# Kernel tuning notes

Measured on AMD Instinct MI355X. Metric: run time of the kernel, lower is better.

The kernel has to match this reference:

```python
import jax, jax.numpy as jnp
import numpy as np

B, H, W, C = 64, 224, 224, 3
P = 16
DIM = 768
DEPTH = 12
NH, DH = 12, 64
FF = 3072
NPATCH = (H // P) * (W // P)   # 196
L = NPATCH + 1                 # 197 tokens (CLS + patches)
KEEP = int(L * (1.0 - 0.75))   # 49 unmasked tokens


def setup_inputs() -> dict:
    key = jax.random.key(0)
    ks = jax.random.split(key, 16)
    s = 0.02
    inp = {
        'inputs': jax.random.normal(ks[0], (B, H, W, C), jnp.float32),
        'conv_w': jax.random.normal(ks[1], (P, P, C, DIM), jnp.float32) * s,
        'ct':     jax.random.normal(ks[2], (1, 1, DIM), jnp.float32) * s,
        'pe':     jax.random.normal(ks[3], (1, L, DIM), jnp.float32) * s,
        'ln1_s': jnp.ones((DEPTH, DIM), jnp.float32),
        'ln1_b': jnp.zeros((DEPTH, DIM), jnp.float32),
        'qkv_w': jax.random.normal(ks[4], (DEPTH, DIM, 3 * NH * DH), jnp.float32) * s,
        'proj_w': jax.random.normal(ks[5], (DEPTH, NH * DH, DIM), jnp.float32) * s,
        'ln2_s': jnp.ones((DEPTH, DIM), jnp.float32),
        'ln2_b': jnp.zeros((DEPTH, DIM), jnp.float32),
        'w1': jax.random.normal(ks[6], (DEPTH, DIM, FF), jnp.float32) * s,
        'b1': jnp.zeros((DEPTH, FF), jnp.float32),
        'w2': jax.random.normal(ks[7], (DEPTH, FF, DIM), jnp.float32) * s,
        'b2': jnp.zeros((DEPTH, DIM), jnp.float32),
        # Faithful to original: permutation of arange(1, L+1); max value 197
        # is out-of-range and gets clamped by JAX gather, exactly as upstream.
        'mask_idx': jax.random.permutation(ks[8], jnp.arange(1, L + 1))[:KEEP].astype(jnp.int32),
    }
    return inp


def _layernorm(x, scale, bias, eps=1e-9):
    m = jnp.mean(x, axis=-1, keepdims=True)
    v = jnp.var(x, axis=-1, keepdims=True)
    return (x - m) * jax.lax.rsqrt(v + eps) * scale + bias


def _encoder(x, layer_params):
    # x: [B, KEEP, DIM]; layer_params leaves stacked on axis 0 (DEPTH)
    inv_sqrt_d = 1.0 / jnp.sqrt(jnp.float32(DH))

    def block(x, p):
        ln1s, ln1b, qw, pw, ln2s, ln2b, w1, b1, w2, b2 = p
        h = _layernorm(x, ln1s, ln1b)
        qkv = h @ qw                                   # [B, Lk, 3*NH*DH]
        q, k, v = jnp.split(qkv, 3, axis=-1)
        def heads(t):
            return t.reshape(x.shape[0], -1, NH, DH).transpose(0, 2, 1, 3)
        q, k, v = heads(q), heads(k), heads(v)         # [B, NH, Lk, DH]
        att = jax.nn.softmax(jnp.einsum('bhqd,bhkd->bhqk', q, k) * inv_sqrt_d)
        o = jnp.einsum('bhqk,bhkd->bhqd', att, v)
        o = o.transpose(0, 2, 1, 3).reshape(x.shape[0], -1, NH * DH) @ pw
        x = x + o
        h2 = _layernorm(x, ln2s, ln2b)
        x = x + (jax.nn.gelu(h2 @ w1 + b1) @ w2 + b2)
        return x, None

    x, _ = jax.lax.scan(block, x, layer_params)
    return x


def reference(inputs, conv_w, ct, pe, ln1_s, ln1_b, qkv_w, proj_w,
              ln2_s, ln2_b, w1, b1, w2, b2, mask_idx):
    # patch embed: stride-P conv, no bias
    out = jax.lax.conv_general_dilated(
        inputs, conv_w, window_strides=(P, P), padding='VALID',
        dimension_numbers=('NHWC', 'HWIO', 'NHWC'))      # [B, 14, 14, DIM]
    out = out.reshape(out.shape[0], -1, out.shape[3])     # [B, 196, DIM]
    out = jnp.concatenate((jnp.repeat(ct, out.shape[0], axis=0), out), axis=1)
    out = out + pe                                        # [B, 197, DIM]
    patches = out[:, mask_idx]                            # [B, 49, DIM]
    layer_params = (ln1_s, ln1_b, qkv_w, proj_w, ln2_s, ln2_b, w1, b1, w2, b2)
    return _encoder(patches, layer_params)
```

## Files before the change

### kernel.cpp

```cpp
#include <hip/hip_runtime.h>
#include <hip/hip_bf16.h>
#include <math.h>

#define DIMV   768
#define BATCH  64
#define KEEPT  49
#define MTOK   (BATCH*KEEPT)
#define NHEADS 12
#define DHEAD  64
#define FFV    3072
#define NDEPTH 12

typedef short short8 __attribute__((ext_vector_type(8)));
typedef float floatx4 __attribute__((ext_vector_type(4)));
typedef unsigned short ushort;

__device__ __forceinline__ ushort f2bf(float f) {
  __hip_bfloat16 h = __float2bfloat16(f);
  return *(ushort*)&h;
}

__device__ __forceinline__ void async_cp16(const void* g, void* l) {
  __builtin_amdgcn_global_load_lds((const __attribute__((address_space(1))) void*)g,
                                   (__attribute__((address_space(3))) void*)l,
                                   16, 0, 0);
}

__global__ __launch_bounds__(256) void gather_patches(
    const float* __restrict__ inp, const int* __restrict__ mask,
    __hip_bfloat16* __restrict__ apix)
{
  int gid = blockIdx.x * 256 + threadIdx.x;
  if (gid >= MTOK * DIMV) return;
  int r = gid / DIMV, k = gid - r * DIMV;
  int b = r / KEEPT, t = r - b * KEEPT;
  int j = mask[t];
  j = j < 0 ? 0 : (j > 196 ? 196 : j);
  float v = 0.f;
  if (j > 0) {
    int p  = j - 1, py = p / 14, px = p - py * 14;
    int ky = k / 48, rem = k - ky * 48, kx = rem / 3, c = rem - kx * 3;
    v = inp[(((b * 224) + py * 16 + ky) * 224 + px * 16 + kx) * 3 + c];
  }
  apix[gid] = __float2bfloat16(v);
}

__global__ __launch_bounds__(256) void finish_embed(
    float* __restrict__ x, const float* __restrict__ ct,
    const float* __restrict__ pe, const int* __restrict__ mask)
{
  int gid = blockIdx.x * 256 + threadIdx.x;
  if (gid >= MTOK * DIMV) return;
  int r = gid / DIMV, d = gid - r * DIMV;
  int t = r % KEEPT;
  int j = mask[t];
  j = j < 0 ? 0 : (j > 196 ? 196 : j);
  float base = (j == 0) ? ct[d] : x[gid];
  x[gid] = base + pe[j * DIMV + d];
}

__global__ __launch_bounds__(256) void layernorm_k(
    const float* __restrict__ x, const float* __restrict__ sc,
    const float* __restrict__ bi, __hip_bfloat16* __restrict__ out)
{
  __shared__ float red[8];
  int r = blockIdx.x;
  const float* xr = x + (size_t)r * DIMV;
  int t = threadIdx.x;
  float v[3];
  float s = 0.f, ss = 0.f;
#pragma unroll
  for (int i = 0; i < 3; i++) {
    float a = xr[t + i * 256];
    v[i] = a; s += a; ss += a * a;
  }
#pragma unroll
  for (int off = 32; off > 0; off >>= 1) {
    s  += __shfl_down(s,  off, 64);
    ss += __shfl_down(ss, off, 64);
  }
  int wave = t >> 6, lane = t & 63;
  if (lane == 0) { red[wave] = s; red[4 + wave] = ss; }
  __syncthreads();
  if (t == 0) {
    float a  = red[0] + red[1] + red[2] + red[3];
    float b2 = red[4] + red[5] + red[6] + red[7];
    float m  = a * (1.f / DIMV);
    float var = b2 * (1.f / DIMV) - m * m;
    red[0] = m;
    red[1] = rsqrtf(var + 1e-9f);
  }
  __syncthreads();
  float m = red[0], rs = red[1];
  __hip_bfloat16* outr = out + (size_t)r * DIMV;
#pragma unroll
  for (int i = 0; i < 3; i++) {
    int d = t + i * 256;
    outr[d] = __float2bfloat16((v[i] - m) * rs * sc[d] + bi[d]);
  }
}

__device__ __forceinline__ void transpose_tile64(
    const float* __restrict__ src, __hip_bfloat16* __restrict__ dst,
    int R, int C, int tr, int tcc)
{
  __shared__ float lds[64][65];
  const int tid = threadIdx.x;
  const int r0 = tr * 64, c0 = tcc * 64;
  const int lr = tid >> 4, lc4 = (tid & 15) * 4;
#pragma unroll
  for (int p = 0; p < 4; p++) {
    float4 v = *(const float4*)(src + (size_t)(r0 + p * 16 + lr) * C + c0 + lc4);
    lds[p * 16 + lr][lc4 + 0] = v.x;
    lds[p * 16 + lr][lc4 + 1] = v.y;
    lds[p * 16 + lr][lc4 + 2] = v.z;
    lds[p * 16 + lr][lc4 + 3] = v.w;
  }
  __syncthreads();
#pragma unroll
  for (int p = 0; p < 4; p++) {
    int c  = p * 16 + (tid >> 4);
    int rc = (tid & 15) * 4;
    ushort4 ov;
    ov.x = f2bf(lds[rc + 0][c]);
    ov.y = f2bf(lds[rc + 1][c]);
    ov.z = f2bf(lds[rc + 2][c]);
    ov.w = f2bf(lds[rc + 3][c]);
    *(ushort4*)((ushort*)dst + (size_t)(c0 + c) * R + r0 + rc) = ov;
  }
}

__global__ __launch_bounds__(256) void transpose_one(
    const float* __restrict__ src, __hip_bfloat16* __restrict__ dst, int R, int C)
{
  int tc = C >> 6;
  transpose_tile64(src, dst, R, C, blockIdx.x / tc, blockIdx.x % tc);
}

#define QKV_TE  ((size_t)2304*768)
#define PROJ_TE ((size_t)768*768)
#define W1_TE   ((size_t)3072*768)
#define W2_TE   ((size_t)768*3072)
#define LSTRIDE (QKV_TE + PROJ_TE + W1_TE + W2_TE)

__global__ __launch_bounds__(256) void convert_weights(
    const float* __restrict__ qkv_w, const float* __restrict__ proj_w,
    const float* __restrict__ w1, const float* __restrict__ w2,
    __hip_bfloat16* __restrict__ dstBase, int layer0, size_t dstStride)
{
  int l = layer0 + blockIdx.y;
  __hip_bfloat16* d = dstBase + (size_t)blockIdx.y * dstStride;
  int tile = blockIdx.x;
  const float* src; __hip_bfloat16* dst; int R, C, t0;
  if (tile < 432)       { src = qkv_w  + (size_t)l*768*2304; dst = d;                          R=768;  C=2304; t0=tile; }
  else if (tile < 576)  { src = proj_w + (size_t)l*768*768;  dst = d + QKV_TE;                 R=768;  C=768;  t0=tile-432; }
  else if (tile < 1152) { src = w1     + (size_t)l*768*3072; dst = d + QKV_TE+PROJ_TE;         R=768;  C=3072; t0=tile-576; }
  else                  { src = w2     + (size_t)l*3072*768; dst = d + QKV_TE+PROJ_TE+W1_TE;   R=3072; C=768;  t0=tile-1152; }
  int tc = C >> 6;
  transpose_tile64(src, dst, R, C, t0 / tc, t0 % tc);
}

enum { EPI_NONE = 0, EPI_RESID = 1, EPI_BIAS_GELU = 2, EPI_BIAS_RESID = 3 };

template <int TN, int EPI, bool OUT_BF16>
__global__ __launch_bounds__(256) void gemm_mfma(
    const ushort* __restrict__ A, const ushort* __restrict__ Bt,
    const float* __restrict__ Cin, const float* __restrict__ bias,
    void* __restrict__ Cout, int M, int N, int K)
{
  constexpr int AM = (TN == 128) ? 4 : 2;
  constexpr int B_LOADS = TN / 64;
  __shared__ ushort As[128 * 32];
  __shared__ ushort Bs[TN * 32];

  const int tid  = threadIdx.x;
  const int wave = tid >> 6, lane = tid & 63;
  const int bm = blockIdx.y, bn = blockIdx.x;

  const int wm0 = (TN == 128) ? (wave & 1) * 64 : wave * 32;
  const int wn0 = (TN == 128) ? (wave >> 1) * 64 : 0;

  floatx4 acc[AM][4];
#pragma unroll
  for (int i = 0; i < AM; i++)
#pragma unroll
    for (int j = 0; j < 4; j++) { floatx4 z = {0.f,0.f,0.f,0.f}; acc[i][j] = z; }

  const int lrow = lane >> 2, lchunk = (lane & 3) * 8;
  const ushort* aSrc[2];
  ushort*       aDst[2];
#pragma unroll
  for (int i = 0; i < 2; i++) {
    int row = bm * 128 + (wave * 2 + i) * 16 + lrow;
    row = row < M - 1 ? row : M - 1;
    aSrc[i] = A + (size_t)row * K + lchunk;
    aDst[i] = As + (wave * 2 + i) * 512;
  }
  const ushort* bSrc[B_LOADS];
  ushort*       bDst[B_LOADS];
#pragma unroll
  for (int i = 0; i < B_LOADS; i++) {
    int row = bn * TN + (wave * B_LOADS + i) * 16 + lrow;
    bSrc[i] = Bt + (size_t)row * K + lchunk;
    bDst[i] = Bs + (wave * B_LOADS + i) * 512;
  }

  for (int k0 = 0; k0 < K; k0 += 32) {
    __syncthreads();
#pragma unroll
    for (int i = 0; i < 2; i++)       async_cp16(aSrc[i] + k0, aDst[i]);
#pragma unroll
    for (int i = 0; i < B_LOADS; i++) async_cp16(bSrc[i] + k0, bDst[i]);
    __syncthreads();

    short8 af[AM], bf[4];
#pragma unroll
    for (int mt = 0; mt < AM; mt++)
      af[mt] = *(const short8*)&As[(wm0 + mt * 16 + (lane & 15)) * 32 + (lane >> 4) * 8];
#pragma unroll
    for (int nt = 0; nt < 4; nt++)
      bf[nt] = *(const short8*)&Bs[(wn0 + nt * 16 + (lane & 15)) * 32 + (lane >> 4) * 8];
#pragma unroll
    for (int mt = 0; mt < AM; mt++)
#pragma unroll
      for (int nt = 0; nt < 4; nt++)
        acc[mt][nt] = __builtin_amdgcn_mfma_f32_16x16x32_bf16(af[mt], bf[nt], acc[mt][nt], 0, 0, 0);
  }

  const int colb = bn * TN + wn0 + (lane & 15);
  const int rq   = (lane >> 4) * 4;
#pragma unroll
  for (int mt = 0; mt < AM; mt++) {
#pragma unroll
    for (int r = 0; r < 4; r++) {
      int row = bm * 128 + wm0 + mt * 16 + rq + r;
      if (row >= M) continue;
#pragma unroll
      for (int nt = 0; nt < 4; nt++) {
        int col = colb + nt * 16;
        float u = acc[mt][nt][r];
        if (EPI == EPI_BIAS_GELU || EPI == EPI_BIAS_RESID) u += bias[col];
        if (EPI == EPI_BIAS_GELU) {
          float t3 = u * u * u;
          u = 0.5f * u * (1.f + tanhf(0.7978845608028654f * (u + 0.044715f * t3)));
        }
        if (EPI == EPI_RESID || EPI == EPI_BIAS_RESID) u += Cin[(size_t)row * N + col];
        if (OUT_BF16)
          ((__hip_bfloat16*)Cout)[(size_t)row * N + col] = __float2bfloat16(u);
        else
          ((float*)Cout)[(size_t)row * N + col] = u;
      }
    }
  }
}

__global__ __launch_bounds__(64) void attn_mfma(
    const ushort* __restrict__ qkv, ushort* __restrict__ o)
{
  __shared__ ushort qA[64 * 72];
  __shared__ ushort kB[64 * 72];
  __shared__ ushort vT[64 * 72];
  __shared__ ushort pA[64 * 72];
  const int b = blockIdx.x, hh = blockIdx.y;
  const int lane = threadIdx.x;
  const int fr = lane & 15, fc = lane >> 4;

  const ushort* base = qkv + (size_t)b * KEEPT * (3 * DIMV) + hh * 64;
  for (int r = 0; r < KEEPT; r++) {
    const ushort* row = base + (size_t)r * (3 * DIMV);
    qA[r * 72 + lane] = row[lane];
    kB[r * 72 + lane] = row[DIMV + lane];
    vT[lane * 72 + r] = row[2 * DIMV + lane];
  }
#pragma unroll
  for (int r = KEEPT; r < 64; r++) {
    qA[r * 72 + lane] = 0;
    kB[r * 72 + lane] = 0;
    vT[lane * 72 + r] = 0;
  }
  __syncthreads();

  floatx4 sacc[4][4];
#pragma unroll
  for (int mt = 0; mt < 4; mt++)
#pragma unroll
    for (int nt = 0; nt < 4; nt++) { floatx4 z = {0.f,0.f,0.f,0.f}; sacc[mt][nt] = z; }

#pragma unroll
  for (int kk = 0; kk < 2; kk++) {
    const int ch = kk * 32 + fc * 8;
    short8 af[4], bf[4];
#pragma unroll
    for (int mt = 0; mt < 4; mt++) af[mt] = *(const short8*)&qA[(mt * 16 + fr) * 72 + ch];
#pragma unroll
    for (int nt = 0; nt < 4; nt++) bf[nt] = *(const short8*)&kB[(nt * 16 + fr) * 72 + ch];
#pragma unroll
    for (int mt = 0; mt < 4; mt++)
#pragma unroll
      for (int nt = 0; nt < 4; nt++)
        sacc[mt][nt] = __builtin_amdgcn_mfma_f32_16x16x32_bf16(af[mt], bf[nt], sacc[mt][nt], 0, 0, 0);
  }

  float inv[4][4];
#pragma unroll
  for (int mt = 0; mt < 4; mt++) {
#pragma unroll
    for (int r = 0; r < 4; r++) {
      float mx = -1e30f;
#pragma unroll
      for (int nt = 0; nt < 4; nt++) {
        float s = sacc[mt][nt][r] * 0.125f;
        if (nt == 3 && fr >= 1) s = -1e30f;
        sacc[mt][nt][r] = s;
        mx = fmaxf(mx, s);
      }
      mx = fmaxf(mx, __shfl_xor(mx, 1, 64));
      mx = fmaxf(mx, __shfl_xor(mx, 2, 64));
      mx = fmaxf(mx, __shfl_xor(mx, 4, 64));
      mx = fmaxf(mx, __shfl_xor(mx, 8, 64));
      float sum = 0.f;
#pragma unroll
      for (int nt = 0; nt < 4; nt++) {
        float e = __expf(sacc[mt][nt][r] - mx);
        sacc[mt][nt][r] = e;
        sum += e;
      }
      sum += __shfl_xor(sum, 1, 64);
      sum += __shfl_xor(sum, 2, 64);
      sum += __shfl_xor(sum, 4, 64);
      sum += __shfl_xor(sum, 8, 64);
      inv[mt][r] = 1.f / sum;
    }
  }

#pragma unroll
  for (int mt = 0; mt < 4; mt++)
#pragma unroll
    for (int r = 0; r < 4; r++)
#pragma unroll
      for (int nt = 0; nt < 4; nt++)
        pA[(mt * 16 + fc * 4 + r) * 72 + nt * 16 + fr] = f2bf(sacc[mt][nt][r]);
  __syncthreads();

  floatx4 oacc[4][4];
#pragma unroll
  for (int mt = 0; mt < 4; mt++)
#pragma unroll
    for (int nt = 0; nt < 4; nt++) { floatx4 z = {0.f,0.f,0.f,0.f}; oacc[mt][nt] = z; }

#pragma unroll
  for (int kk = 0; kk < 2; kk++) {
    const int ch = kk * 32 + fc * 8;
    short8 af[4], bf[4];
#pragma unroll
    for (int mt = 0; mt < 4; mt++) af[mt] = *(const short8*)&pA[(mt * 16 + fr) * 72 + ch];
#pragma unroll
    for (int nt = 0; nt < 4; nt++) bf[nt] = *(const short8*)&vT[(nt * 16 + fr) * 72 + ch];
#pragma unroll
    for (int mt = 0; mt < 4; mt++)
#pragma unroll
      for (int nt = 0; nt < 4; nt++)
        oacc[mt][nt] = __builtin_amdgcn_mfma_f32_16x16x32_bf16(af[mt], bf[nt], oacc[mt][nt], 0, 0, 0);
  }

  ushort* obase = o + (size_t)b * KEEPT * DIMV + hh * 64;
#pragma unroll
  for (int mt = 0; mt < 4; mt++)
#pragma unroll
    for (int r = 0; r < 4; r++) {
      int q = mt * 16 + fc * 4 + r;
      if (q < KEEPT) {
#pragma unroll
        for (int nt = 0; nt < 4; nt++)
          obase[(size_t)q * DIMV + nt * 16 + fr] = f2bf(oacc[mt][nt][r] * inv[mt][r]);
      }
    }
}

extern "C" void kernel_launch(void* const* d_in, const int* in_sizes, int n_in,
                              void* d_out, int out_size, void* d_ws, size_t ws_size,
                              hipStream_t stream)
{
  (void)in_sizes; (void)n_in; (void)out_size;
  const float* inputs = (const float*)d_in[0];
  const float* conv_w = (const float*)d_in[1];
  const float* ct     = (const float*)d_in[2];
  const float* pe     = (const float*)d_in[3];
  const float* ln1_s  = (const float*)d_in[4];
  const float* ln1_b  = (const float*)d_in[5];
  const float* qkv_w  = (const float*)d_in[6];
  const float* proj_w = (const float*)d_in[7];
  const float* ln2_s  = (const float*)d_in[8];
  const float* ln2_b  = (const float*)d_in[9];
  const float* w1     = (const float*)d_in[10];
  const float* b1     = (const float*)d_in[11];
  const float* w2     = (const float*)d_in[12];
  const float* b2     = (const float*)d_in[13];
  const int*   mask   = (const int*)d_in[14];
  float* out = (float*)d_out;

  char* wsb = (char*)d_ws;
  float*          x     = (float*)wsb;
  __hip_bfloat16* h     = (__hip_bfloat16*)(wsb + 9633792);
  __hip_bfloat16* big   = (__hip_bfloat16*)(wsb + 9633792 + 4816896);
  __hip_bfloat16* convT = (__hip_bfloat16*)(wsb + 9633792 + 4816896 + 19267584);
  __hip_bfloat16* wbuf  = (__hip_bfloat16*)(wsb + 9633792 + 4816896 + 19267584 + 1179648);
  const size_t base_bytes = 9633792ull + 4816896 + 19267584 + 1179648;
  const bool all_mode = ws_size >= base_bytes + 12ull * LSTRIDE * 2;

  __hip_bfloat16* apix = h;
  __hip_bfloat16* qkv  = big;
  __hip_bfloat16* g    = big;

  dim3 blk(256);
  const int nelem = MTOK * DIMV;
  const int nblk  = (nelem + 255) / 256;
  const int mg    = (MTOK + 127) / 128;

  transpose_one<<<144, blk, 0, stream>>>(conv_w, convT, 768, 768);
  if (all_mode)
    convert_weights<<<dim3(1728, 12), blk, 0, stream>>>(
        qkv_w, proj_w, w1, w2, wbuf, 0, LSTRIDE);

  gather_patches<<<nblk, blk, 0, stream>>>(inputs, mask, apix);
  gemm_mfma<64, EPI_NONE, false><<<dim3(12, mg), blk, 0, stream>>>(
      (const ushort*)apix, (const ushort*)convT, nullptr, nullptr, x,
      MTOK, DIMV, DIMV);
  finish_embed<<<nblk, blk, 0, stream>>>(x, ct, pe, mask);

  for (int l = 0; l < NDEPTH; l++) {
    __hip_bfloat16* wl = wbuf + (all_mode ? (size_t)l * LSTRIDE : 0);
    if (!all_mode)
      convert_weights<<<dim3(1728, 1), blk, 0, stream>>>(
          qkv_w, proj_w, w1, w2, wbuf, l, 0);
    const ushort* qkvT  = (const ushort*)wl;
    const ushort* projT = (const ushort*)(wl + QKV_TE);
    const ushort* w1T   = (const ushort*)(wl + QKV_TE + PROJ_TE);
    const ushort* w2T   = (const ushort*)(wl + QKV_TE + PROJ_TE + W1_TE);

    layernorm_k<<<MTOK, blk, 0, stream>>>(x, ln1_s + l * DIMV, ln1_b + l * DIMV, h);
    gemm_mfma<128, EPI_NONE, true><<<dim3(18, mg), blk, 0, stream>>>(
        (const ushort*)h, qkvT, nullptr, nullptr, qkv, MTOK, 3 * DIMV, DIMV);
    attn_mfma<<<dim3(BATCH, NHEADS), dim3(64), 0, stream>>>(
        (const ushort*)qkv, (ushort*)h);
    gemm_mfma<64, EPI_RESID, false><<<dim3(12, mg), blk, 0, stream>>>(
        (const ushort*)h, projT, x, nullptr, x, MTOK, DIMV, DIMV);
    layernorm_k<<<MTOK, blk, 0, stream>>>(x, ln2_s + l * DIMV, ln2_b + l * DIMV, h);
    gemm_mfma<128, EPI_BIAS_GELU, true><<<dim3(24, mg), blk, 0, stream>>>(
        (const ushort*)h, w1T, nullptr, b1 + (size_t)l * FFV, g, MTOK, FFV, DIMV);
    float* dst = (l == NDEPTH - 1) ? out : x;
    gemm_mfma<64, EPI_BIAS_RESID, false><<<dim3(12, mg), blk, 0, stream>>>(
        (const ushort*)g, w2T, x, b2 + (size_t)l * DIMV, dst, MTOK, DIMV, FFV);
  }
}
```

Baseline: 2.492 ms.

## Split attention across four waves, fuse embed epilogue, widen transpose stores

The attention kernel now runs 256 threads per (batch, head) block. Each wave owns 16 query rows, and Q/K are loaded into LDS with vectorized 16-byte loads, which is meant to raise occupancy and cut serial per-lane loads. The finish_embed pass is folded into the patch-embedding GEMM epilogue (CLS/pos-embed add), removing one full read/write of x and a launch. The weight transpose now writes 16-byte vectors instead of 8-byte ones, at the cost of more strided LDS column reads per thread.

```diff
diff --git a/kernel.cpp b/kernel.cpp
--- a/kernel.cpp
+++ b/kernel.cpp
@@ -14,6 +14,7 @@
 typedef short short8 __attribute__((ext_vector_type(8)));
 typedef float floatx4 __attribute__((ext_vector_type(4)));
 typedef unsigned short ushort;
+typedef unsigned short ushortx8 __attribute__((ext_vector_type(8)));
 
 __device__ __forceinline__ ushort f2bf(float f) {
   __hip_bfloat16 h = __float2bfloat16(f);
@@ -45,20 +46,6 @@
   apix[gid] = __float2bfloat16(v);
 }
 
-__global__ __launch_bounds__(256) void finish_embed(
-    float* __restrict__ x, const float* __restrict__ ct,
-    const float* __restrict__ pe, const int* __restrict__ mask)
-{
-  int gid = blockIdx.x * 256 + threadIdx.x;
-  if (gid >= MTOK * DIMV) return;
-  int r = gid / DIMV, d = gid - r * DIMV;
-  int t = r % KEEPT;
-  int j = mask[t];
-  j = j < 0 ? 0 : (j > 196 ? 196 : j);
-  float base = (j == 0) ? ct[d] : x[gid];
-  x[gid] = base + pe[j * DIMV + d];
-}
-
 __global__ __launch_bounds__(256) void layernorm_k(
     const float* __restrict__ x, const float* __restrict__ sc,
     const float* __restrict__ bi, __hip_bfloat16* __restrict__ out)
@@ -117,17 +104,15 @@
     lds[p * 16 + lr][lc4 + 3] = v.w;
   }
   __syncthreads();
-#pragma unroll
-  for (int p = 0; p < 4; p++) {
-    int c  = p * 16 + (tid >> 4);
-    int rc = (tid & 15) * 4;
-    ushort4 ov;
-    ov.x = f2bf(lds[rc + 0][c]);
-    ov.y = f2bf(lds[rc + 1][c]);
-    ov.z = f2bf(lds[rc + 2][c]);
-    ov.w = f2bf(lds[rc + 3][c]);
-    *(ushort4*)((ushort*)dst + (size_t)(c0 + c) * R + r0 + rc) = ov;
-  }
+  const int c = tid >> 2, rc = (tid & 3) * 8;
+  ushortx8 o0, o1;
+#pragma unroll
+  for (int j = 0; j < 8; j++) o0[j] = f2bf(lds[rc + j][c]);
+#pragma unroll
+  for (int j = 0; j < 8; j++) o1[j] = f2bf(lds[rc + 32 + j][c]);
+  ushort* drow = (ushort*)dst + (size_t)(c0 + c) * R + r0;
+  *(ushortx8*)(drow + rc)      = o0;
+  *(ushortx8*)(drow + rc + 32) = o1;
 }
 
 __global__ __launch_bounds__(256) void transpose_one(
@@ -160,12 +145,14 @@
   transpose_tile64(src, dst, R, C, t0 / tc, t0 % tc);
 }
 
-enum { EPI_NONE = 0, EPI_RESID = 1, EPI_BIAS_GELU = 2, EPI_BIAS_RESID = 3 };
+enum { EPI_NONE = 0, EPI_RESID = 1, EPI_BIAS_GELU = 2, EPI_BIAS_RESID = 3,
+       EPI_EMBED = 4 };
 
 template <int TN, int EPI, bool OUT_BF16>
 __global__ __launch_bounds__(256) void gemm_mfma(
     const ushort* __restrict__ A, const ushort* __restrict__ Bt,
     const float* __restrict__ Cin, const float* __restrict__ bias,
+    const float* __restrict__ pe, const int* __restrict__ mask,
     void* __restrict__ Cout, int M, int N, int K)
 {
   constexpr int AM = (TN == 128) ? 4 : 2;
@@ -245,6 +232,13 @@
           u = 0.5f * u * (1.f + tanhf(0.7978845608028654f * (u + 0.044715f * t3)));
         }
         if (EPI == EPI_RESID || EPI == EPI_BIAS_RESID) u += Cin[(size_t)row * N + col];
+        if (EPI == EPI_EMBED) {
+          int t = row % KEEPT;
+          int j = mask[t];
+          j = j < 0 ? 0 : (j > 196 ? 196 : j);
+          if (j == 0) u = bias[col];
+          u += pe[(size_t)j * DIMV + col];
+        }
         if (OUT_BF16)
           ((__hip_bfloat16*)Cout)[(size_t)row * N + col] = __float2bfloat16(u);
         else
@@ -254,7 +248,7 @@
   }
 }
 
-__global__ __launch_bounds__(64) void attn_mfma(
+__global__ __launch_bounds__(256) void attn_mfma(
     const ushort* __restrict__ qkv, ushort* __restrict__ o)
 {
   __shared__ ushort qA[64 * 72];
@@ -262,119 +256,110 @@
   __shared__ ushort vT[64 * 72];
   __shared__ ushort pA[64 * 72];
   const int b = blockIdx.x, hh = blockIdx.y;
-  const int lane = threadIdx.x;
+  const int tid = threadIdx.x;
+  const int wave = tid >> 6, lane = tid & 63;
   const int fr = lane & 15, fc = lane >> 4;
 
   const ushort* base = qkv + (size_t)b * KEEPT * (3 * DIMV) + hh * 64;
-  for (int r = 0; r < KEEPT; r++) {
-    const ushort* row = base + (size_t)r * (3 * DIMV);
-    qA[r * 72 + lane] = row[lane];
-    kB[r * 72 + lane] = row[DIMV + lane];
-    vT[lane * 72 + r] = row[2 * DIMV + lane];
-  }
-#pragma unroll
-  for (int r = KEEPT; r < 64; r++) {
-    qA[r * 72 + lane] = 0;
-    kB[r * 72 + lane] = 0;
-    vT[lane * 72 + r] = 0;
+
+#pragma unroll
+  for (int it = 0; it < 2; it++) {
+    int r  = it * 32 + wave * 8 + (lane >> 3);
+    int cc = (lane & 7) * 8;
+    short8 qv = {0,0,0,0,0,0,0,0};
+    short8 kv = {0,0,0,0,0,0,0,0};
+    if (r < KEEPT) {
+      const ushort* row = base + (size_t)r * (3 * DIMV);
+      qv = *(const short8*)(row + cc);
+      kv = *(const short8*)(row + DIMV + cc);
+    }
+    *(short8*)&qA[r * 72 + cc] = qv;
+    *(short8*)&kB[r * 72 + cc] = kv;
+  }
+  for (int r = wave; r < 64; r += 4) {
+    ushort v = 0;
+    if (r < KEEPT) v = base[(size_t)r * (3 * DIMV) + 2 * DIMV + lane];
+    vT[lane * 72 + r] = v;
   }
   __syncthreads();
 
-  floatx4 sacc[4][4];
-#pragma unroll
-  for (int mt = 0; mt < 4; mt++)
-#pragma unroll
-    for (int nt = 0; nt < 4; nt++) { floatx4 z = {0.f,0.f,0.f,0.f}; sacc[mt][nt] = z; }
+  const int q0 = wave * 16;
+  floatx4 sacc[4];
+#pragma unroll
+  for (int nt = 0; nt < 4; nt++) { floatx4 z = {0.f,0.f,0.f,0.f}; sacc[nt] = z; }
 
 #pragma unroll
   for (int kk = 0; kk < 2; kk++) {
     const int ch = kk * 32 + fc * 8;
-    short8 af[4], bf[4];
-#pragma unroll
-    for (int mt = 0; mt < 4; mt++) af[mt] = *(const short8*)&qA[(mt * 16 + fr) * 72 + ch];
-#pragma unroll
-    for (int nt = 0; nt < 4; nt++) bf[nt] = *(const short8*)&kB[(nt * 16 + fr) * 72 + ch];
-#pragma unroll
-    for (int mt = 0; mt < 4; mt++)
-#pragma unroll
-      for (int nt = 0; nt < 4; nt++)
-        sacc[mt][nt] = __builtin_amdgcn_mfma_f32_16x16x32_bf16(af[mt], bf[nt], sacc[mt][nt], 0, 0, 0);
-  }
-
-  float inv[4][4];
-#pragma unroll
-  for (int mt = 0; mt < 4; mt++) {
-#pragma unroll
-    for (int r = 0; r < 4; r++) {
-      float mx = -1e30f;
-#pragma unroll
-      for (int nt = 0; nt < 4; nt++) {
-        float s = sacc[mt][nt][r] * 0.125f;
-        if (nt == 3 && fr >= 1) s = -1e30f;
-        sacc[mt][nt][r] = s;
-        mx = fmaxf(mx, s);
-      }
-      mx = fmaxf(mx, __shfl_xor(mx, 1, 64));
-      mx = fmaxf(mx, __shfl_xor(mx, 2, 64));
-      mx = fmaxf(mx, __shfl_xor(mx, 4, 64));
-      mx = fmaxf(mx, __shfl_xor(mx, 8, 64));
-      float sum = 0.f;
-#pragma unroll
-      for (int nt = 0; nt < 4; nt++) {
-        float e = __expf(sacc[mt][nt][r] - mx);
-        sacc[mt][nt][r] = e;
-        sum += e;
-      }
-      sum += __shfl_xor(sum, 1, 64);
-      sum += __shfl_xor(sum, 2, 64);
-      sum += __shfl_xor(sum, 4, 64);
-      sum += __shfl_xor(sum, 8, 64);
-      inv[mt][r] = 1.f / sum;
-    }
-  }
-
-#pragma unroll
-  for (int mt = 0; mt < 4; mt++)
-#pragma unroll
-    for (int r = 0; r < 4; r++)
-#pragma unroll
-      for (int nt = 0; nt < 4; nt++)
-        pA[(mt * 16 + fc * 4 + r) * 72 + nt * 16 + fr] = f2bf(sacc[mt][nt][r]);
+    short8 af = *(const short8*)&qA[(q0 + fr) * 72 + ch];
+#pragma unroll
+    for (int nt = 0; nt < 4; nt++) {
+      short8 bf = *(const short8*)&kB[(nt * 16 + fr) * 72 + ch];
+      sacc[nt] = __builtin_amdgcn_mfma_f32_16x16x32_bf16(af, bf, sacc[nt], 0, 0, 0);
+    }
+  }
+
+  float inv[4];
+#pragma unroll
+  for (int r = 0; r < 4; r++) {
+    float mx = -1e30f;
+#pragma unroll
+    for (int nt = 0; nt < 4; nt++) {
+      float s = sacc[nt][r] * 0.125f;
+      if (nt == 3 && fr >= 1) s = -1e30f;
+      sacc[nt][r] = s;
+      mx = fmaxf(mx, s);
+    }
+    mx = fmaxf(mx, __shfl_xor(mx, 1, 64));
+    mx = fmaxf(mx, __shfl_xor(mx, 2, 64));
+    mx = fmaxf(mx, __shfl_xor(mx, 4, 64));
+    mx = fmaxf(mx, __shfl_xor(mx, 8, 64));
+    float sum = 0.f;
+#pragma unroll
+    for (int nt = 0; nt < 4; nt++) {
+      float e = __expf(sacc[nt][r] - mx);
+      sacc[nt][r] = e;
+      sum += e;
+    }
+    sum += __shfl_xor(sum, 1, 64);
+    sum += __shfl_xor(sum, 2, 64);
+    sum += __shfl_xor(sum, 4, 64);
+    sum += __shfl_xor(sum, 8, 64);
+    inv[r] = 1.f / sum;
+  }
+
+#pragma unroll
+  for (int r = 0; r < 4; r++)
+#pragma unroll
+    for (int nt = 0; nt < 4; nt++)
+      pA[(q0 + fc * 4 + r) * 72 + nt * 16 + fr] = f2bf(sacc[nt][r]);
   __syncthreads();
 
-  floatx4 oacc[4][4];
-#pragma unroll
-  for (int mt = 0; mt < 4; mt++)
-#pragma unroll
-    for (int nt = 0; nt < 4; nt++) { floatx4 z = {0.f,0.f,0.f,0.f}; oacc[mt][nt] = z; }
+  floatx4 oacc[4];
+#pragma unroll
+  for (int nt = 0; nt < 4; nt++) { floatx4 z = {0.f,0.f,0.f,0.f}; oacc[nt] = z; }
 
 #pragma unroll
   for (int kk = 0; kk < 2; kk++) {
     const int ch = kk * 32 + fc * 8;
-    short8 af[4], bf[4];
-#pragma unroll
-    for (int mt = 0; mt < 4; mt++) af[mt] = *(const short8*)&pA[(mt * 16 + fr) * 72 + ch];
-#pragma unroll
-    for (int nt = 0; nt < 4; nt++) bf[nt] = *(const short8*)&vT[(nt * 16 + fr) * 72 + ch];
-#pragma unroll
-    for (int mt = 0; mt < 4; mt++)
+    short8 af = *(const short8*)&pA[(q0 + fr) * 72 + ch];
+#pragma unroll
+    for (int nt = 0; nt < 4; nt++) {
+      short8 bf = *(const short8*)&vT[(nt * 16 + fr) * 72 + ch];
+      oacc[nt] = __builtin_amdgcn_mfma_f32_16x16x32_bf16(af, bf, oacc[nt], 0, 0, 0);
+    }
+  }
+
+  ushort* obase = o + (size_t)b * KEEPT * DIMV + hh * 64;
+#pragma unroll
+  for (int r = 0; r < 4; r++) {
+    int q = q0 + fc * 4 + r;
+    if (q < KEEPT) {
 #pragma unroll
       for (int nt = 0; nt < 4; nt++)
-        oacc[mt][nt] = __builtin_amdgcn_mfma_f32_16x16x32_bf16(af[mt], bf[nt], oacc[mt][nt], 0, 0, 0);
-  }
-
-  ushort* obase = o + (size_t)b * KEEPT * DIMV + hh * 64;
-#pragma unroll
-  for (int mt = 0; mt < 4; mt++)
-#pragma unroll
-    for (int r = 0; r < 4; r++) {
-      int q = mt * 16 + fc * 4 + r;
-      if (q < KEEPT) {
-#pragma unroll
-        for (int nt = 0; nt < 4; nt++)
-          obase[(size_t)q * DIMV + nt * 16 + fr] = f2bf(oacc[mt][nt][r] * inv[mt][r]);
-      }
-    }
+        obase[(size_t)q * DIMV + nt * 16 + fr] = f2bf(oacc[nt][r] * inv[r]);
+    }
+  }
 }
 
 extern "C" void kernel_launch(void* const* d_in, const int* in_sizes, int n_in,
@@ -423,10 +408,9 @@
         qkv_w, proj_w, w1, w2, wbuf, 0, LSTRIDE);
 
   gather_patches<<<nblk, blk, 0, stream>>>(inputs, mask, apix);
-  gemm_mfma<64, EPI_NONE, false><<<dim3(12, mg), blk, 0, stream>>>(
-      (const ushort*)apix, (const ushort*)convT, nullptr, nullptr, x,
+  gemm_mfma<64, EPI_EMBED, false><<<dim3(12, mg), blk, 0, stream>>>(
+      (const ushort*)apix, (const ushort*)convT, nullptr, ct, pe, mask, x,
       MTOK, DIMV, DIMV);
-  finish_embed<<<nblk, blk, 0, stream>>>(x, ct, pe, mask);
 
   for (int l = 0; l < NDEPTH; l++) {
     __hip_bfloat16* wl = wbuf + (all_mode ? (size_t)l * LSTRIDE : 0);
@@ -440,16 +424,20 @@
 
     layernorm_k<<<MTOK, blk, 0, stream>>>(x, ln1_s + l * DIMV, ln1_b + l * DIMV, h);
     gemm_mfma<128, EPI_NONE, true><<<dim3(18, mg), blk, 0, stream>>>(
-        (const ushort*)h, qkvT, nullptr, nullptr, qkv, MTOK, 3 * DIMV, DIMV);
-    attn_mfma<<<dim3(BATCH, NHEADS), dim3(64), 0, stream>>>(
+        (const ushort*)h, qkvT, nullptr, nullptr, nullptr, nullptr, qkv,
+        MTOK, 3 * DIMV, DIMV);
+    attn_mfma<<<dim3(BATCH, NHEADS), blk, 0, stream>>>(
         (const ushort*)qkv, (ushort*)h);
     gemm_mfma<64, EPI_RESID, false><<<dim3(12, mg), blk, 0, stream>>>(
-        (const ushort*)h, projT, x, nullptr, x, MTOK, DIMV, DIMV);
+        (const ushort*)h, projT, x, nullptr, nullptr, nullptr, x,
+        MTOK, DIMV, DIMV);
     layernorm_k<<<MTOK, blk, 0, stream>>>(x, ln2_s + l * DIMV, ln2_b + l * DIMV, h);
     gemm_mfma<128, EPI_BIAS_GELU, true><<<dim3(24, mg), blk, 0, stream>>>(
-        (const ushort*)h, w1T, nullptr, b1 + (size_t)l * FFV, g, MTOK, FFV, DIMV);
+        (const ushort*)h, w1T, nullptr, b1 + (size_t)l * FFV, nullptr, nullptr, g,
+        MTOK, FFV, DIMV);
     float* dst = (l == NDEPTH - 1) ? out : x;
     gemm_mfma<64, EPI_BIAS_RESID, false><<<dim3(12, mg), blk, 0, stream>>>(
-        (const ushort*)g, w2T, x, b2 + (size_t)l * DIMV, dst, MTOK, DIMV, FFV);
-  }
-}
+        (const ushort*)g, w2T, x, b2 + (size_t)l * DIMV, nullptr, nullptr, dst,
+        MTOK, DIMV, FFV);
+  }
+}
```

New measurement: 2.495 ms. Within noise of the previous version (+0.1%).
